# Kernel tuning notes

Measured on AMD Instinct MI355X. Metric: run time of the kernel, lower is better.

The kernel has to match this reference:

```python
import jax, jax.numpy as jnp
import numpy as np

B, C, H, W, N = 8, 128, 128, 256, 1024
E1_LAMDA = 1.0
E2_LAMDA = 2.0 / 7.0
EPS = 1e-9


def bilinear_sample(fmap, xs):
    """fmap: (B,C,H,W); xs: (B,N,2) with (x,y) pixel coords -> (B*N, C)."""
    Wd, Hd = fmap.shape[3], fmap.shape[2]
    x = jnp.clip(xs[..., 0], 0.0, Wd - 1.0)
    y = jnp.clip(xs[..., 1], 0.0, Hd - 1.0)
    x0 = jnp.clip(jnp.floor(x).astype(jnp.int32), 0, Wd - 2)
    y0 = jnp.clip(jnp.floor(y).astype(jnp.int32), 0, Hd - 2)
    x1, y1 = x0 + 1, y0 + 1
    wx = (x - x0)[..., None]  # (B,N,1)
    wy = (y - y0)[..., None]
    bidx = jnp.arange(fmap.shape[0])[:, None]  # (B,1) broadcasts with (B,N)
    f00 = fmap[bidx, :, y0, x0]  # (B,N,C)
    f01 = fmap[bidx, :, y0, x1]
    f10 = fmap[bidx, :, y1, x0]
    f11 = fmap[bidx, :, y1, x1]
    out = (f00 * (1 - wx) * (1 - wy) + f01 * wx * (1 - wy)
           + f10 * (1 - wx) * wy + f11 * wx * wy)
    return out.reshape(-1, fmap.shape[1])  # (B*N, C)


def setup_inputs() -> dict:
    key = jax.random.key(0)
    k1, k2, k3, k4 = jax.random.split(key, 4)
    fb = jax.random.normal(k1, (B, C, H, W), dtype=jnp.float32)
    # positive match coords (x in [1,W-2], y in [1,H-2]) so noise stays in-bounds-ish
    ub = jax.random.uniform(k2, (B, N, 2), dtype=jnp.float32) \
         * jnp.array([W - 3.0, H - 3.0], jnp.float32) + 1.0
    noise = jax.random.uniform(k3, (B, N, 2), dtype=jnp.float32, minval=-1.0, maxval=1.0)
    f_t = jax.random.normal(k4, (B * N, C), dtype=jnp.float32)
    return {"fb": fb, "f_t": f_t, "ub": ub, "noise": noise}


def reference(fb, f_t, ub, noise):
    xs = ub + noise                                   # perturbed sample points (B,N,2)
    f_s = bilinear_sample(fb, xs)                     # (BN, C)
    r = f_s - f_t                                     # residual
    # np.gradient-style central differences (one-sided at edges)
    gx = jnp.gradient(fb, axis=3)
    gy = jnp.gradient(fb, axis=2)
    Jx = bilinear_sample(gx, xs)                      # (BN, C)
    Jy = bilinear_sample(gy, xs)
    J = jnp.stack([Jx, Jy], axis=-1)                  # (BN, C, 2)
    Hm = jnp.einsum('nci,ncj->nij', J, J) + EPS * jnp.eye(2, dtype=fb.dtype)
    b = jnp.einsum('nci,nc->ni', J, r)                # (BN, 2)
    # analytic 2x2 inverse
    a_, b_, c_, d_ = Hm[:, 0, 0], Hm[:, 0, 1], Hm[:, 1, 0], Hm[:, 1, 1]
    det = a_ * d_ - b_ * c_
    Hinv = jnp.stack([jnp.stack([d_, -b_], -1),
                      jnp.stack([-c_, a_], -1)], -2) / det[:, None, None]
    miu = xs.reshape(-1, 2) - jnp.einsum('nij,nj->ni', Hinv, b)  # (BN, 2)
    diff = ub.reshape(-1, 2) - miu
    e1 = 0.5 * jnp.sum(jnp.einsum('ni,nij,nj->n', diff, Hm, diff))
    det_c = jnp.clip(det, 1e-16, None)
    e2 = (B * N) * jnp.log(jnp.asarray(2.0 * np.pi, fb.dtype)) - 0.5 * jnp.sum(jnp.log(det_c))
    e = E1_LAMDA * e1 + E2_LAMDA * e2
    return (e, e1, e2)
```

## Files before the change

kernel.cpp:

```cpp
#include <hip/hip_runtime.h>

#define Bq 8
#define Cq 128
#define Hq 128
#define Wq 256
#define Nq 1024
#define BN (Bq * Nq)

#define LOG_2PI 1.8378770664093453f
#define EPSq 1e-9f

__global__ __launch_bounds__(128) void gn_sample_kernel(
    const float* __restrict__ fb,
    const float* __restrict__ f_t,
    const float* __restrict__ ub,
    const float* __restrict__ noise,
    float* __restrict__ ws)
{
    const int n = blockIdx.x;
    const int b = n >> 10;
    const int c = threadIdx.x;

    const float ubx = ub[2 * n];
    const float uby = ub[2 * n + 1];
    const float xsx = ubx + noise[2 * n];
    const float xsy = uby + noise[2 * n + 1];

    float x = fminf(fmaxf(xsx, 0.0f), (float)(Wq - 1));
    float y = fminf(fmaxf(xsy, 0.0f), (float)(Hq - 1));
    int x0 = (int)floorf(x); x0 = min(max(x0, 0), Wq - 2);
    int y0 = (int)floorf(y); y0 = min(max(y0, 0), Hq - 2);
    const int x1 = x0 + 1, y1 = y0 + 1;
    const float wx = x - (float)x0;
    const float wy = y - (float)y0;

    const int xlo0 = max(x0 - 1, 0);
    const int xhi1 = min(x1 + 1, Wq - 1);
    const int ylo0 = max(y0 - 1, 0);
    const int yhi1 = min(y1 + 1, Hq - 1);
    const float sx0 = 1.0f / (float)(x1 - xlo0);
    const float sx1 = 1.0f / (float)(xhi1 - x0);
    const float sy0 = 1.0f / (float)(y1 - ylo0);
    const float sy1 = 1.0f / (float)(yhi1 - y0);

    const float* base = fb + (((size_t)b * Cq + c) * Hq) * Wq;
    const float* rlo = base + (size_t)ylo0 * Wq;
    const float* r0  = base + (size_t)y0  * Wq;
    const float* r1  = base + (size_t)y1  * Wq;
    const float* rhi = base + (size_t)yhi1 * Wq;

    const float f_lo0 = rlo[x0], f_lo1 = rlo[x1];
    const float f0m = r0[xlo0], f00 = r0[x0], f01 = r0[x1], f0p = r0[xhi1];
    const float f1m = r1[xlo0], f10 = r1[x0], f11 = r1[x1], f1p = r1[xhi1];
    const float f_hi0 = rhi[x0], f_hi1 = rhi[x1];

    const float gx00 = (f01 - f0m) * sx0;
    const float gx01 = (f0p - f00) * sx1;
    const float gx10 = (f11 - f1m) * sx0;
    const float gx11 = (f1p - f10) * sx1;
    const float gy00 = (f10 - f_lo0) * sy0;
    const float gy01 = (f11 - f_lo1) * sy0;
    const float gy10 = (f_hi0 - f00) * sy1;
    const float gy11 = (f_hi1 - f01) * sy1;

    const float w00 = (1.0f - wx) * (1.0f - wy);
    const float w01 = wx * (1.0f - wy);
    const float w10 = (1.0f - wx) * wy;
    const float w11 = wx * wy;

    const float fs = f00 * w00 + f01 * w01 + f10 * w10 + f11 * w11;
    const float Jx = gx00 * w00 + gx01 * w01 + gx10 * w10 + gx11 * w11;
    const float Jy = gy00 * w00 + gy01 * w01 + gy10 * w10 + gy11 * w11;
    const float r  = fs - f_t[(size_t)n * Cq + c];

    float hxx = Jx * Jx;
    float hxy = Jx * Jy;
    float hyy = Jy * Jy;
    float bx  = Jx * r;
    float by  = Jy * r;

    #pragma unroll
    for (int off = 32; off > 0; off >>= 1) {
        hxx += __shfl_down(hxx, off);
        hxy += __shfl_down(hxy, off);
        hyy += __shfl_down(hyy, off);
        bx  += __shfl_down(bx, off);
        by  += __shfl_down(by, off);
    }
    __shared__ float red[2][5];
    const int wave = threadIdx.x >> 6;
    if ((threadIdx.x & 63) == 0) {
        red[wave][0] = hxx; red[wave][1] = hxy; red[wave][2] = hyy;
        red[wave][3] = bx;  red[wave][4] = by;
    }
    __syncthreads();
    if (threadIdx.x == 0) {
        const float A  = red[0][0] + red[1][0] + EPSq;
        const float Bv = red[0][1] + red[1][1];
        const float D  = red[0][2] + red[1][2] + EPSq;
        const float bxs = red[0][3] + red[1][3];
        const float bys = red[0][4] + red[1][4];

        const float det = A * D - Bv * Bv;
        const float inv = 1.0f / det;
        const float hbx = ( D * bxs - Bv * bys) * inv;
        const float hby = (-Bv * bxs + A * bys) * inv;
        const float dx = ubx - (xsx - hbx);
        const float dy = uby - (xsy - hby);
        const float quad = A * dx * dx + 2.0f * Bv * dx * dy + D * dy * dy;

        const float detc = fmaxf(det, 1e-16f);
        ws[n]      = 0.5f * quad;
        ws[BN + n] = logf(detc);
    }
}

__global__ __launch_bounds__(1024) void gn_reduce_kernel(
    const float* __restrict__ ws, float* __restrict__ out)
{
    float s1 = 0.0f, s2 = 0.0f;
    for (int i = threadIdx.x; i < BN; i += 1024) {
        s1 += ws[i];
        s2 += ws[BN + i];
    }
    #pragma unroll
    for (int off = 32; off > 0; off >>= 1) {
        s1 += __shfl_down(s1, off);
        s2 += __shfl_down(s2, off);
    }
    __shared__ float l1[16], l2[16];
    const int w = threadIdx.x >> 6;
    if ((threadIdx.x & 63) == 0) { l1[w] = s1; l2[w] = s2; }
    __syncthreads();
    if (threadIdx.x == 0) {
        float e1 = 0.0f, sl = 0.0f;
        #pragma unroll
        for (int i = 0; i < 16; ++i) { e1 += l1[i]; sl += l2[i]; }
        const float e2 = (float)BN * LOG_2PI - 0.5f * sl;
        out[0] = e1 + (2.0f / 7.0f) * e2;
        out[1] = e1;
        out[2] = e2;
    }
}

extern "C" void kernel_launch(void* const* d_in, const int* in_sizes, int n_in,
                              void* d_out, int out_size, void* d_ws, size_t ws_size,
                              hipStream_t stream) {
    const float* fb    = (const float*)d_in[0];
    const float* f_t   = (const float*)d_in[1];
    const float* ub    = (const float*)d_in[2];
    const float* noise = (const float*)d_in[3];
    float* out = (float*)d_out;
    float* ws  = (float*)d_ws;

    gn_sample_kernel<<<BN, 128, 0, stream>>>(fb, f_t, ub, noise, ws);
    gn_reduce_kernel<<<1, 1024, 0, stream>>>(ws, out);
}
```

Before: 217.6 us.

## Transpose feature map to NHWC before sampling for coalesced channel loads

Adds a tiled NCHW-to-NHWC transpose kernel into workspace, then samples with one 64-lane wave per point loading float2 channel pairs contiguously. This replaces per-channel strided scattered reads with coalesced loads and drops the cross-wave shared-memory reduction. In exchange it adds a full read and write pass over the feature map every call, plus workspace use.

```diff
diff --git a/kernel.cpp b/kernel.cpp
--- a/kernel.cpp
+++ b/kernel.cpp
@@ -6,20 +6,50 @@
 #define Wq 256
 #define Nq 1024
 #define BN (Bq * Nq)
+#define HWq (Hq * Wq)
+#define FBT_ELEMS ((size_t)Bq * Cq * HWq)
 
 #define LOG_2PI 1.8378770664093453f
 #define EPSq 1e-9f
 
-__global__ __launch_bounds__(128) void gn_sample_kernel(
-    const float* __restrict__ fb,
+__global__ __launch_bounds__(256) void transpose_nchw_nhwc(
+    const float* __restrict__ in, float* __restrict__ out)
+{
+    __shared__ float tile[64][65];
+    const int blk = blockIdx.x;
+    const int ct = blk & 1;
+    const int pt = (blk >> 1) & 511;
+    const int b  = blk >> 10;
+    const int c0 = ct << 6;
+    const int p0 = pt << 6;
+    const int tx = threadIdx.x & 63;
+    const int ty = threadIdx.x >> 6;
+
+    const float* src = in + ((size_t)b * Cq + c0) * HWq + p0;
+    #pragma unroll
+    for (int i = 0; i < 16; ++i) {
+        const int cy = ty + (i << 2);
+        tile[cy][tx] = src[(size_t)cy * HWq + tx];
+    }
+    __syncthreads();
+    float* dst = out + ((size_t)b * HWq + p0) * Cq + c0;
+    #pragma unroll
+    for (int i = 0; i < 16; ++i) {
+        const int py = ty + (i << 2);
+        dst[(size_t)py * Cq + tx] = tile[tx][py];
+    }
+}
+
+__global__ __launch_bounds__(64) void gn_sample_nhwc(
+    const float* __restrict__ fbT,
     const float* __restrict__ f_t,
     const float* __restrict__ ub,
     const float* __restrict__ noise,
-    float* __restrict__ ws)
+    float* __restrict__ partials)
 {
     const int n = blockIdx.x;
     const int b = n >> 10;
-    const int c = threadIdx.x;
+    const int lane = threadIdx.x;
 
     const float ubx = ub[2 * n];
     const float uby = ub[2 * n + 1];
@@ -43,41 +73,54 @@
     const float sy0 = 1.0f / (float)(y1 - ylo0);
     const float sy1 = 1.0f / (float)(yhi1 - y0);
 
-    const float* base = fb + (((size_t)b * Cq + c) * Hq) * Wq;
-    const float* rlo = base + (size_t)ylo0 * Wq;
-    const float* r0  = base + (size_t)y0  * Wq;
-    const float* r1  = base + (size_t)y1  * Wq;
-    const float* rhi = base + (size_t)yhi1 * Wq;
+    const size_t bb = (size_t)b * HWq;
+    const int co = lane * 2;
+    #define PT(yy, xx) (*(const float2*)(fbT + ((bb + (size_t)(yy) * Wq + (xx)) * Cq + co)))
 
-    const float f_lo0 = rlo[x0], f_lo1 = rlo[x1];
-    const float f0m = r0[xlo0], f00 = r0[x0], f01 = r0[x1], f0p = r0[xhi1];
-    const float f1m = r1[xlo0], f10 = r1[x0], f11 = r1[x1], f1p = r1[xhi1];
-    const float f_hi0 = rhi[x0], f_hi1 = rhi[x1];
+    const float2 f_lo0 = PT(ylo0, x0), f_lo1 = PT(ylo0, x1);
+    const float2 f0m = PT(y0, xlo0), f00 = PT(y0, x0), f01 = PT(y0, x1), f0p = PT(y0, xhi1);
+    const float2 f1m = PT(y1, xlo0), f10 = PT(y1, x0), f11 = PT(y1, x1), f1p = PT(y1, xhi1);
+    const float2 f_hi0 = PT(yhi1, x0), f_hi1 = PT(yhi1, x1);
+    #undef PT
 
-    const float gx00 = (f01 - f0m) * sx0;
-    const float gx01 = (f0p - f00) * sx1;
-    const float gx10 = (f11 - f1m) * sx0;
-    const float gx11 = (f1p - f10) * sx1;
-    const float gy00 = (f10 - f_lo0) * sy0;
-    const float gy01 = (f11 - f_lo1) * sy0;
-    const float gy10 = (f_hi0 - f00) * sy1;
-    const float gy11 = (f_hi1 - f01) * sy1;
+    const float2 ft = *(const float2*)(f_t + (size_t)n * Cq + co);
 
     const float w00 = (1.0f - wx) * (1.0f - wy);
     const float w01 = wx * (1.0f - wy);
     const float w10 = (1.0f - wx) * wy;
     const float w11 = wx * wy;
 
-    const float fs = f00 * w00 + f01 * w01 + f10 * w10 + f11 * w11;
-    const float Jx = gx00 * w00 + gx01 * w01 + gx10 * w10 + gx11 * w11;
-    const float Jy = gy00 * w00 + gy01 * w01 + gy10 * w10 + gy11 * w11;
-    const float r  = fs - f_t[(size_t)n * Cq + c];
+    float hxx = 0.0f, hxy = 0.0f, hyy = 0.0f, bx = 0.0f, by = 0.0f;
+    #pragma unroll
+    for (int k = 0; k < 2; ++k) {
+        const float vlo0 = (k ? f_lo0.y : f_lo0.x), vlo1 = (k ? f_lo1.y : f_lo1.x);
+        const float v0m = (k ? f0m.y : f0m.x), v00 = (k ? f00.y : f00.x);
+        const float v01 = (k ? f01.y : f01.x), v0p = (k ? f0p.y : f0p.x);
+        const float v1m = (k ? f1m.y : f1m.x), v10 = (k ? f10.y : f10.x);
+        const float v11 = (k ? f11.y : f11.x), v1p = (k ? f1p.y : f1p.x);
+        const float vhi0 = (k ? f_hi0.y : f_hi0.x), vhi1 = (k ? f_hi1.y : f_hi1.x);
+        const float vt = (k ? ft.y : ft.x);
 
-    float hxx = Jx * Jx;
-    float hxy = Jx * Jy;
-    float hyy = Jy * Jy;
-    float bx  = Jx * r;
-    float by  = Jy * r;
+        const float gx00 = (v01 - v0m) * sx0;
+        const float gx01 = (v0p - v00) * sx1;
+        const float gx10 = (v11 - v1m) * sx0;
+        const float gx11 = (v1p - v10) * sx1;
+        const float gy00 = (v10 - vlo0) * sy0;
+        const float gy01 = (v11 - vlo1) * sy0;
+        const float gy10 = (vhi0 - v00) * sy1;
+        const float gy11 = (vhi1 - v01) * sy1;
+
+        const float fs = v00 * w00 + v01 * w01 + v10 * w10 + v11 * w11;
+        const float Jx = gx00 * w00 + gx01 * w01 + gx10 * w10 + gx11 * w11;
+        const float Jy = gy00 * w00 + gy01 * w01 + gy10 * w10 + gy11 * w11;
+        const float r  = fs - vt;
+
+        hxx += Jx * Jx;
+        hxy += Jx * Jy;
+        hyy += Jy * Jy;
+        bx  += Jx * r;
+        by  += Jy * r;
+    }
 
     #pragma unroll
     for (int off = 32; off > 0; off >>= 1) {
@@ -87,41 +130,33 @@
         bx  += __shfl_down(bx, off);
         by  += __shfl_down(by, off);
     }
-    __shared__ float red[2][5];
-    const int wave = threadIdx.x >> 6;
-    if ((threadIdx.x & 63) == 0) {
-        red[wave][0] = hxx; red[wave][1] = hxy; red[wave][2] = hyy;
-        red[wave][3] = bx;  red[wave][4] = by;
-    }
-    __syncthreads();
-    if (threadIdx.x == 0) {
-        const float A  = red[0][0] + red[1][0] + EPSq;
-        const float Bv = red[0][1] + red[1][1];
-        const float D  = red[0][2] + red[1][2] + EPSq;
-        const float bxs = red[0][3] + red[1][3];
-        const float bys = red[0][4] + red[1][4];
+
+    if (lane == 0) {
+        const float A  = hxx + EPSq;
+        const float Bv = hxy;
+        const float D  = hyy + EPSq;
 
         const float det = A * D - Bv * Bv;
         const float inv = 1.0f / det;
-        const float hbx = ( D * bxs - Bv * bys) * inv;
-        const float hby = (-Bv * bxs + A * bys) * inv;
+        const float hbx = ( D * bx - Bv * by) * inv;
+        const float hby = (-Bv * bx + A * by) * inv;
         const float dx = ubx - (xsx - hbx);
         const float dy = uby - (xsy - hby);
         const float quad = A * dx * dx + 2.0f * Bv * dx * dy + D * dy * dy;
 
         const float detc = fmaxf(det, 1e-16f);
-        ws[n]      = 0.5f * quad;
-        ws[BN + n] = logf(detc);
+        partials[n]      = 0.5f * quad;
+        partials[BN + n] = logf(detc);
     }
 }
 
 __global__ __launch_bounds__(1024) void gn_reduce_kernel(
-    const float* __restrict__ ws, float* __restrict__ out)
+    const float* __restrict__ partials, float* __restrict__ out)
 {
     float s1 = 0.0f, s2 = 0.0f;
     for (int i = threadIdx.x; i < BN; i += 1024) {
-        s1 += ws[i];
-        s2 += ws[BN + i];
+        s1 += partials[i];
+        s2 += partials[BN + i];
     }
     #pragma unroll
     for (int off = 32; off > 0; off >>= 1) {
@@ -151,8 +186,11 @@
     const float* ub    = (const float*)d_in[2];
     const float* noise = (const float*)d_in[3];
     float* out = (float*)d_out;
-    float* ws  = (float*)d_ws;
+    float* wsf = (float*)d_ws;
+    float* fbT      = wsf;
+    float* partials = wsf + FBT_ELEMS;
 
-    gn_sample_kernel<<<BN, 128, 0, stream>>>(fb, f_t, ub, noise, ws);
-    gn_reduce_kernel<<<1, 1024, 0, stream>>>(ws, out);
+    transpose_nchw_nhwc<<<Bq * (HWq / 64) * (Cq / 64), 256, 0, stream>>>(fb, fbT);
+    gn_sample_nhwc<<<BN, 64, 0, stream>>>(fbT, f_t, ub, noise, partials);
+    gn_reduce_kernel<<<1, 1024, 0, stream>>>(partials, out);
 }
```

Result: slower. 233.8 us (+7.4%).

## Bin sample points by row band and stage feature rows through LDS tiles

Applied to the files above, without the earlier changes.

Sample points are bucketed per batch into 4-row bands using an atomic binning pass. Each block then loads an 8-row by 8-channel slab of the feature map into shared memory with coalesced float4 reads, and evaluates every point in its bin from that tile. Per-chunk partial Hessians and gradients are written out, and a separate kernel combines them, solves the 2x2 system and hands off to the final reduction. This swaps strided per-channel gathers from global memory for streaming the whole feature map, about twice over, plus extra launches and intermediate traffic.

```diff
diff --git a/kernel.cpp b/kernel.cpp
--- a/kernel.cpp
+++ b/kernel.cpp
@@ -6,122 +6,199 @@
 #define Wq 256
 #define Nq 1024
 #define BN (Bq * Nq)
+#define HWq (Hq * Wq)
 
 #define LOG_2PI 1.8378770664093453f
 #define EPSq 1e-9f
 
-__global__ __launch_bounds__(128) void gn_sample_kernel(
+#define NGRP 32
+#define NBINS (Bq * NGRP)
+#define BIN_CAP 1024
+#define CCH 8
+#define NCHUNK (Cq / CCH)
+
+#define BS_OFF 256
+#define H_OFF (BS_OFF + NBINS * BIN_CAP)
+#define P2_OFF (H_OFF + NCHUNK * BN * 5)
+
+__global__ void zero_bins(int* __restrict__ bc) { bc[threadIdx.x] = 0; }
+
+__global__ __launch_bounds__(256) void binprep(
+    const float* __restrict__ ub, const float* __restrict__ noise,
+    int* __restrict__ bc, int* __restrict__ bs)
+{
+    const int n = blockIdx.x * 256 + threadIdx.x;
+    const float xsy = ub[2 * n + 1] + noise[2 * n + 1];
+    float y = fminf(fmaxf(xsy, 0.0f), (float)(Hq - 1));
+    int y0 = (int)floorf(y); y0 = min(max(y0, 0), Hq - 2);
+    const int g = (y0 == 0) ? 0 : ((y0 - 1) >> 2);
+    const int bin = (n >> 10) * NGRP + g;
+    const int idx = atomicAdd(&bc[bin], 1);
+    if (idx < BIN_CAP) bs[bin * BIN_CAP + idx] = n;
+}
+
+__global__ __launch_bounds__(512) void gn_binned(
     const float* __restrict__ fb,
     const float* __restrict__ f_t,
     const float* __restrict__ ub,
     const float* __restrict__ noise,
-    float* __restrict__ ws)
-{
-    const int n = blockIdx.x;
-    const int b = n >> 10;
-    const int c = threadIdx.x;
+    const int* __restrict__ bc,
+    const int* __restrict__ bs,
+    float* __restrict__ pH)
+{
+    __shared__ float tile[8 * 256 * 9];
+    const int blk  = blockIdx.x;
+    const int bin  = blk >> 4;
+    const int chunk = blk & 15;
+    const int b = bin >> 5;
+    const int g = bin & 31;
+    const int t = threadIdx.x;
+
+    {
+        const int cr = t >> 3;
+        const int i  = cr >> 3;
+        const int c  = cr & 7;
+        const int fq = t & 7;
+        const int row = min(4 * g + i, Hq - 1);
+        const float* src = fb +
+            (((size_t)b * Cq + chunk * CCH + c) * Hq + row) * Wq;
+        #pragma unroll
+        for (int k = 0; k < 8; ++k) {
+            const int f4 = fq + 8 * k;
+            const float4 v = *(const float4*)(src + 4 * f4);
+            const int px = 4 * f4;
+            tile[(i * 256 + px + 0) * 9 + c] = v.x;
+            tile[(i * 256 + px + 1) * 9 + c] = v.y;
+            tile[(i * 256 + px + 2) * 9 + c] = v.z;
+            tile[(i * 256 + px + 3) * 9 + c] = v.w;
+        }
+    }
+    __syncthreads();
+
+    const int nb = bc[bin];
+    const int group = t >> 3;
+    const int lc = t & 7;
+    const int ch = chunk * CCH + lc;
+
+    for (int s = group; s < nb; s += 64) {
+        const int n = bs[bin * BIN_CAP + s];
+
+        const float xsx = ub[2 * n]     + noise[2 * n];
+        const float xsy = ub[2 * n + 1] + noise[2 * n + 1];
+
+        float x = fminf(fmaxf(xsx, 0.0f), (float)(Wq - 1));
+        float y = fminf(fmaxf(xsy, 0.0f), (float)(Hq - 1));
+        int x0 = (int)floorf(x); x0 = min(max(x0, 0), Wq - 2);
+        int y0 = (int)floorf(y); y0 = min(max(y0, 0), Hq - 2);
+        const int x1 = x0 + 1, y1 = y0 + 1;
+        const float wx = x - (float)x0;
+        const float wy = y - (float)y0;
+
+        const int xlo0 = max(x0 - 1, 0);
+        const int xhi1 = min(x1 + 1, Wq - 1);
+        const int ylo0 = max(y0 - 1, 0);
+        const int yhi1 = min(y1 + 1, Hq - 1);
+        const float sx0 = 1.0f / (float)(x1 - xlo0);
+        const float sx1 = 1.0f / (float)(xhi1 - x0);
+        const float sy0 = 1.0f / (float)(y1 - ylo0);
+        const float sy1 = 1.0f / (float)(yhi1 - y0);
+
+        const int ilo = ylo0 - 4 * g;
+        const int i0  = y0   - 4 * g;
+        const int i1  = i0 + 1;
+        const int ihi = yhi1 - 4 * g;
+
+        #define LD(ii, xx) tile[((ii) * 256 + (xx)) * 9 + lc]
+        const float f_lo0 = LD(ilo, x0), f_lo1 = LD(ilo, x1);
+        const float f0m = LD(i0, xlo0), f00 = LD(i0, x0);
+        const float f01 = LD(i0, x1),   f0p = LD(i0, xhi1);
+        const float f1m = LD(i1, xlo0), f10 = LD(i1, x0);
+        const float f11 = LD(i1, x1),   f1p = LD(i1, xhi1);
+        const float f_hi0 = LD(ihi, x0), f_hi1 = LD(ihi, x1);
+        #undef LD
+
+        const float gx00 = (f01 - f0m) * sx0;
+        const float gx01 = (f0p - f00) * sx1;
+        const float gx10 = (f11 - f1m) * sx0;
+        const float gx11 = (f1p - f10) * sx1;
+        const float gy00 = (f10 - f_lo0) * sy0;
+        const float gy01 = (f11 - f_lo1) * sy0;
+        const float gy10 = (f_hi0 - f00) * sy1;
+        const float gy11 = (f_hi1 - f01) * sy1;
+
+        const float w00 = (1.0f - wx) * (1.0f - wy);
+        const float w01 = wx * (1.0f - wy);
+        const float w10 = (1.0f - wx) * wy;
+        const float w11 = wx * wy;
+
+        const float fs = f00 * w00 + f01 * w01 + f10 * w10 + f11 * w11;
+        const float Jx = gx00 * w00 + gx01 * w01 + gx10 * w10 + gx11 * w11;
+        const float Jy = gy00 * w00 + gy01 * w01 + gy10 * w10 + gy11 * w11;
+        const float r  = fs - f_t[(size_t)n * Cq + ch];
+
+        float hxx = Jx * Jx;
+        float hxy = Jx * Jy;
+        float hyy = Jy * Jy;
+        float bx  = Jx * r;
+        float by  = Jy * r;
+
+        #pragma unroll
+        for (int off = 1; off < 8; off <<= 1) {
+            hxx += __shfl_xor(hxx, off);
+            hxy += __shfl_xor(hxy, off);
+            hyy += __shfl_xor(hyy, off);
+            bx  += __shfl_xor(bx, off);
+            by  += __shfl_xor(by, off);
+        }
+        if (lc == 0) {
+            float* o = pH + ((size_t)chunk * BN + n) * 5;
+            o[0] = hxx; o[1] = hxy; o[2] = hyy; o[3] = bx; o[4] = by;
+        }
+    }
+}
+
+__global__ __launch_bounds__(256) void gn_finalA(
+    const float* __restrict__ pH,
+    const float* __restrict__ ub, const float* __restrict__ noise,
+    float* __restrict__ p2)
+{
+    const int n = blockIdx.x * 256 + threadIdx.x;
+    float hxx = 0.0f, hxy = 0.0f, hyy = 0.0f, bx = 0.0f, by = 0.0f;
+    #pragma unroll
+    for (int k = 0; k < NCHUNK; ++k) {
+        const float* o = pH + ((size_t)k * BN + n) * 5;
+        hxx += o[0]; hxy += o[1]; hyy += o[2]; bx += o[3]; by += o[4];
+    }
 
     const float ubx = ub[2 * n];
     const float uby = ub[2 * n + 1];
     const float xsx = ubx + noise[2 * n];
     const float xsy = uby + noise[2 * n + 1];
 
-    float x = fminf(fmaxf(xsx, 0.0f), (float)(Wq - 1));
-    float y = fminf(fmaxf(xsy, 0.0f), (float)(Hq - 1));
-    int x0 = (int)floorf(x); x0 = min(max(x0, 0), Wq - 2);
-    int y0 = (int)floorf(y); y0 = min(max(y0, 0), Hq - 2);
-    const int x1 = x0 + 1, y1 = y0 + 1;
-    const float wx = x - (float)x0;
-    const float wy = y - (float)y0;
-
-    const int xlo0 = max(x0 - 1, 0);
-    const int xhi1 = min(x1 + 1, Wq - 1);
-    const int ylo0 = max(y0 - 1, 0);
-    const int yhi1 = min(y1 + 1, Hq - 1);
-    const float sx0 = 1.0f / (float)(x1 - xlo0);
-    const float sx1 = 1.0f / (float)(xhi1 - x0);
-    const float sy0 = 1.0f / (float)(y1 - ylo0);
-    const float sy1 = 1.0f / (float)(yhi1 - y0);
-
-    const float* base = fb + (((size_t)b * Cq + c) * Hq) * Wq;
-    const float* rlo = base + (size_t)ylo0 * Wq;
-    const float* r0  = base + (size_t)y0  * Wq;
-    const float* r1  = base + (size_t)y1  * Wq;
-    const float* rhi = base + (size_t)yhi1 * Wq;
-
-    const float f_lo0 = rlo[x0], f_lo1 = rlo[x1];
-    const float f0m = r0[xlo0], f00 = r0[x0], f01 = r0[x1], f0p = r0[xhi1];
-    const float f1m = r1[xlo0], f10 = r1[x0], f11 = r1[x1], f1p = r1[xhi1];
-    const float f_hi0 = rhi[x0], f_hi1 = rhi[x1];
-
-    const float gx00 = (f01 - f0m) * sx0;
-    const float gx01 = (f0p - f00) * sx1;
-    const float gx10 = (f11 - f1m) * sx0;
-    const float gx11 = (f1p - f10) * sx1;
-    const float gy00 = (f10 - f_lo0) * sy0;
-    const float gy01 = (f11 - f_lo1) * sy0;
-    const float gy10 = (f_hi0 - f00) * sy1;
-    const float gy11 = (f_hi1 - f01) * sy1;
-
-    const float w00 = (1.0f - wx) * (1.0f - wy);
-    const float w01 = wx * (1.0f - wy);
-    const float w10 = (1.0f - wx) * wy;
-    const float w11 = wx * wy;
-
-    const float fs = f00 * w00 + f01 * w01 + f10 * w10 + f11 * w11;
-    const float Jx = gx00 * w00 + gx01 * w01 + gx10 * w10 + gx11 * w11;
-    const float Jy = gy00 * w00 + gy01 * w01 + gy10 * w10 + gy11 * w11;
-    const float r  = fs - f_t[(size_t)n * Cq + c];
-
-    float hxx = Jx * Jx;
-    float hxy = Jx * Jy;
-    float hyy = Jy * Jy;
-    float bx  = Jx * r;
-    float by  = Jy * r;
-
-    #pragma unroll
-    for (int off = 32; off > 0; off >>= 1) {
-        hxx += __shfl_down(hxx, off);
-        hxy += __shfl_down(hxy, off);
-        hyy += __shfl_down(hyy, off);
-        bx  += __shfl_down(bx, off);
-        by  += __shfl_down(by, off);
-    }
-    __shared__ float red[2][5];
-    const int wave = threadIdx.x >> 6;
-    if ((threadIdx.x & 63) == 0) {
-        red[wave][0] = hxx; red[wave][1] = hxy; red[wave][2] = hyy;
-        red[wave][3] = bx;  red[wave][4] = by;
-    }
-    __syncthreads();
-    if (threadIdx.x == 0) {
-        const float A  = red[0][0] + red[1][0] + EPSq;
-        const float Bv = red[0][1] + red[1][1];
-        const float D  = red[0][2] + red[1][2] + EPSq;
-        const float bxs = red[0][3] + red[1][3];
-        const float bys = red[0][4] + red[1][4];
-
-        const float det = A * D - Bv * Bv;
-        const float inv = 1.0f / det;
-        const float hbx = ( D * bxs - Bv * bys) * inv;
-        const float hby = (-Bv * bxs + A * bys) * inv;
-        const float dx = ubx - (xsx - hbx);
-        const float dy = uby - (xsy - hby);
-        const float quad = A * dx * dx + 2.0f * Bv * dx * dy + D * dy * dy;
-
-        const float detc = fmaxf(det, 1e-16f);
-        ws[n]      = 0.5f * quad;
-        ws[BN + n] = logf(detc);
-    }
+    const float A  = hxx + EPSq;
+    const float Bv = hxy;
+    const float D  = hyy + EPSq;
+
+    const float det = A * D - Bv * Bv;
+    const float inv = 1.0f / det;
+    const float hbx = ( D * bx - Bv * by) * inv;
+    const float hby = (-Bv * bx + A * by) * inv;
+    const float dx = ubx - (xsx - hbx);
+    const float dy = uby - (xsy - hby);
+    const float quad = A * dx * dx + 2.0f * Bv * dx * dy + D * dy * dy;
+
+    const float detc = fmaxf(det, 1e-16f);
+    p2[n]      = 0.5f * quad;
+    p2[BN + n] = logf(detc);
 }
 
 __global__ __launch_bounds__(1024) void gn_reduce_kernel(
-    const float* __restrict__ ws, float* __restrict__ out)
+    const float* __restrict__ p2, float* __restrict__ out)
 {
     float s1 = 0.0f, s2 = 0.0f;
     for (int i = threadIdx.x; i < BN; i += 1024) {
-        s1 += ws[i];
-        s2 += ws[BN + i];
+        s1 += p2[i];
+        s2 += p2[BN + i];
     }
     #pragma unroll
     for (int off = 32; off > 0; off >>= 1) {
@@ -151,8 +228,17 @@
     const float* ub    = (const float*)d_in[2];
     const float* noise = (const float*)d_in[3];
     float* out = (float*)d_out;
-    float* ws  = (float*)d_ws;
-
-    gn_sample_kernel<<<BN, 128, 0, stream>>>(fb, f_t, ub, noise, ws);
-    gn_reduce_kernel<<<1, 1024, 0, stream>>>(ws, out);
-}
+    int*   wsi = (int*)d_ws;
+    float* wsf = (float*)d_ws;
+
+    int*   bc = wsi;
+    int*   bs = wsi + BS_OFF;
+    float* pH = wsf + H_OFF;
+    float* p2 = wsf + P2_OFF;
+
+    zero_bins<<<1, NBINS, 0, stream>>>(bc);
+    binprep<<<BN / 256, 256, 0, stream>>>(ub, noise, bc, bs);
+    gn_binned<<<NBINS * NCHUNK, 512, 0, stream>>>(fb, f_t, ub, noise, bc, bs, pH);
+    gn_finalA<<<BN / 256, 256, 0, stream>>>(pH, ub, noise, p2);
+    gn_reduce_kernel<<<1, 1024, 0, stream>>>(p2, out);
+}
```

Measured after the change: 212.7 us (median of 2 runs). 2.3% less time.

## Bin sample points by image row band to improve cache locality of gathers

Applied to the files above, without the earlier changes.

Adds preprocessing kernels that group sample points into bins by batch and a 4-row band of y, then flatten the bins into a processing order so the main gather kernel visits points with nearby rows consecutively. The aim is more L2/MALL reuse of the feature-map rows that neighbouring blocks read. In exchange it adds three small launches, global atomics and an extra indirection. Atomic ordering within a bin is nondeterministic, but the final sums do not depend on that order beyond float rounding.

```diff
diff --git a/kernel.cpp b/kernel.cpp
--- a/kernel.cpp
+++ b/kernel.cpp
@@ -6,25 +6,66 @@
 #define Wq 256
 #define Nq 1024
 #define BN (Bq * Nq)
+#define HWq (Hq * Wq)
 
 #define LOG_2PI 1.8378770664093453f
 #define EPSq 1e-9f
 
-__global__ __launch_bounds__(128) void gn_sample_kernel(
+#define NGRP 32
+#define NBINS (Bq * NGRP)
+#define BIN_CAP 1024
+
+#define BS_OFF 256
+#define ORDER_OFF (BS_OFF + NBINS * BIN_CAP)
+#define GEOM_OFF (ORDER_OFF + BN)
+#define P2_OFF  (GEOM_OFF + BN * 2)
+
+__global__ void zero_bins(int* __restrict__ bc) { bc[threadIdx.x] = 0; }
+
+__global__ __launch_bounds__(256) void binprep(
+    const float* __restrict__ ub, const float* __restrict__ noise,
+    int* __restrict__ bc, int* __restrict__ bs, float* __restrict__ geom)
+{
+    const int n = blockIdx.x * 256 + threadIdx.x;
+    const float2 u  = ((const float2*)ub)[n];
+    const float2 nz = ((const float2*)noise)[n];
+    const float xsx = u.x + nz.x;
+    const float xsy = u.y + nz.y;
+    ((float2*)geom)[n] = make_float2(xsx, xsy);
+
+    float y = fminf(fmaxf(xsy, 0.0f), (float)(Hq - 1));
+    int y0 = (int)floorf(y); y0 = min(max(y0, 0), Hq - 2);
+    const int bin = (n >> 10) * NGRP + (y0 >> 2);
+    const int idx = atomicAdd(&bc[bin], 1);
+    bs[bin * BIN_CAP + idx] = n;
+}
+
+__global__ __launch_bounds__(64) void flatten(
+    const int* __restrict__ bc, const int* __restrict__ bs,
+    int* __restrict__ order)
+{
+    const int bin = blockIdx.x;
+    int start = 0;
+    for (int k = 0; k < bin; ++k) start += bc[k];
+    const int nb = bc[bin];
+    for (int j = threadIdx.x; j < nb; j += 64)
+        order[start + j] = bs[bin * BIN_CAP + j];
+}
+
+__global__ __launch_bounds__(128) void gn_direct(
     const float* __restrict__ fb,
     const float* __restrict__ f_t,
     const float* __restrict__ ub,
-    const float* __restrict__ noise,
-    float* __restrict__ ws)
-{
-    const int n = blockIdx.x;
+    const int* __restrict__ order,
+    const float* __restrict__ geom,
+    float* __restrict__ p2)
+{
+    const int n = order[blockIdx.x];
     const int b = n >> 10;
     const int c = threadIdx.x;
 
-    const float ubx = ub[2 * n];
-    const float uby = ub[2 * n + 1];
-    const float xsx = ubx + noise[2 * n];
-    const float xsy = uby + noise[2 * n + 1];
+    const float2 xs = ((const float2*)geom)[n];
+    const float xsx = xs.x, xsy = xs.y;
 
     float x = fminf(fmaxf(xsx, 0.0f), (float)(Wq - 1));
     float y = fminf(fmaxf(xsy, 0.0f), (float)(Hq - 1));
@@ -105,23 +146,25 @@
         const float inv = 1.0f / det;
         const float hbx = ( D * bxs - Bv * bys) * inv;
         const float hby = (-Bv * bxs + A * bys) * inv;
+        const float ubx = ub[2 * n];
+        const float uby = ub[2 * n + 1];
         const float dx = ubx - (xsx - hbx);
         const float dy = uby - (xsy - hby);
         const float quad = A * dx * dx + 2.0f * Bv * dx * dy + D * dy * dy;
 
         const float detc = fmaxf(det, 1e-16f);
-        ws[n]      = 0.5f * quad;
-        ws[BN + n] = logf(detc);
+        p2[n]      = 0.5f * quad;
+        p2[BN + n] = logf(detc);
     }
 }
 
 __global__ __launch_bounds__(1024) void gn_reduce_kernel(
-    const float* __restrict__ ws, float* __restrict__ out)
+    const float* __restrict__ p2, float* __restrict__ out)
 {
     float s1 = 0.0f, s2 = 0.0f;
     for (int i = threadIdx.x; i < BN; i += 1024) {
-        s1 += ws[i];
-        s2 += ws[BN + i];
+        s1 += p2[i];
+        s2 += p2[BN + i];
     }
     #pragma unroll
     for (int off = 32; off > 0; off >>= 1) {
@@ -151,8 +194,18 @@
     const float* ub    = (const float*)d_in[2];
     const float* noise = (const float*)d_in[3];
     float* out = (float*)d_out;
-    float* ws  = (float*)d_ws;
-
-    gn_sample_kernel<<<BN, 128, 0, stream>>>(fb, f_t, ub, noise, ws);
-    gn_reduce_kernel<<<1, 1024, 0, stream>>>(ws, out);
-}
+    int*   wsi = (int*)d_ws;
+    float* wsf = (float*)d_ws;
+
+    int*   bc    = wsi;
+    int*   bs    = wsi + BS_OFF;
+    int*   order = wsi + ORDER_OFF;
+    float* geom  = wsf + GEOM_OFF;
+    float* p2    = wsf + P2_OFF;
+
+    zero_bins<<<1, NBINS, 0, stream>>>(bc);
+    binprep<<<BN / 256, 256, 0, stream>>>(ub, noise, bc, bs, geom);
+    flatten<<<NBINS, 64, 0, stream>>>(bc, bs, order);
+    gn_direct<<<BN, 128, 0, stream>>>(fb, f_t, ub, order, geom, p2);
+    gn_reduce_kernel<<<1, 1024, 0, stream>>>(p2, out);
+}
```

Result: slower. 231.2 us (+6.2%).
